# Kernel tuning notes

Hardware: AMD Instinct MI355X
Metric: run time of the kernel (lower is better)

## Reference

```python
import jax, jax.numpy as jnp
import numpy as np

D_MODEL, D_HEAD, N_HEAD, PERIOD = 1024, 64, 16, 30
B, T1, T2 = 2, 2048, 2048


def setup_inputs() -> dict:
    key = jax.random.key(0)
    ks = jax.random.split(key, 7)
    s_in = 1.0 / np.sqrt(D_MODEL)
    s_out = 1.0 / np.sqrt(N_HEAD * D_HEAD)
    return {
        "x": jax.random.normal(ks[0], (B, T1, D_MODEL), dtype=jnp.float32),
        "context": jax.random.normal(ks[1], (B, T2, D_MODEL), dtype=jnp.float32),
        "Wq": jax.random.uniform(ks[2], (N_HEAD * D_HEAD, D_MODEL), jnp.float32, -s_in, s_in),
        "Wk": jax.random.uniform(ks[3], (N_HEAD * D_HEAD, D_MODEL), jnp.float32, -s_in, s_in),
        "Wv": jax.random.uniform(ks[4], (N_HEAD * D_HEAD, D_MODEL), jnp.float32, -s_in, s_in),
        "Wo": jax.random.uniform(ks[5], (D_MODEL, N_HEAD * D_HEAD), jnp.float32, -s_out, s_out),
        "bo": jax.random.uniform(ks[6], (D_MODEL,), jnp.float32, -s_out, s_out),
    }


def reference(x, context, Wq, Wk, Wv, Wo, bo):
    Bx, T1x, _ = x.shape
    T2x = context.shape[1]
    scale = 1.0 / np.sqrt(D_HEAD).astype(np.float32)
    # projections (torch Linear: y = x @ W^T)
    q = (x @ Wq.T).reshape(Bx, T1x, N_HEAD, D_HEAD)
    k = (context @ Wk.T).reshape(Bx, T2x, N_HEAD, D_HEAD)
    v = (context @ Wv.T).reshape(Bx, T2x, N_HEAD, D_HEAD)
    # attention scores [B, H, T1, T2]
    scores = jnp.einsum('bihd,bjhd->bhij', q, k) * scale
    # ALiBi-style periodic distance bias
    dist = jnp.abs(jnp.arange(T1x)[:, None] - jnp.arange(T2x)[None, :])  # [T1,T2]
    bias = -(dist // PERIOD).astype(jnp.float32)                          # [T1,T2]
    head_scale = jnp.power(2.0, -jnp.arange(1, N_HEAD + 1, dtype=jnp.float32))
    biased = scores + bias[None, None, :, :] * head_scale[None, :, None, None]
    attn = jax.nn.softmax(biased, axis=-1)
    out = jnp.einsum('bhij,bjhd->bihd', attn, v).reshape(Bx, T1x, N_HEAD * D_HEAD)
    # output projection; dropout is identity in eval mode
    return out @ Wo.T + bo
```

## Files before the change

### kernel.cpp

```cpp
#include <hip/hip_runtime.h>
#include <hip/hip_fp16.h>

typedef _Float16 f16;
typedef __attribute__((ext_vector_type(8))) _Float16 f16x8;
typedef __attribute__((ext_vector_type(4))) _Float16 f16x4;
typedef __attribute__((ext_vector_type(2))) __fp16 fp16x2;
typedef __attribute__((ext_vector_type(4))) float f32x4;
typedef __attribute__((ext_vector_type(16))) float f32x16;

#define DM 1024
#define NH 16
#define DH 64
#define TT 2048
#define LOG2E 1.4426950408889634f
#define QSCALE 0.18033688f

__device__ __forceinline__ void gl16(const void* g, void* l) {
  __builtin_amdgcn_global_load_lds((const __attribute__((address_space(1))) void*)g,
                                   (__attribute__((address_space(3))) void*)l, 16, 0, 0);
}

#define SB0 __builtin_amdgcn_sched_barrier(0)
#define LGKM0 asm volatile("s_waitcnt lgkmcnt(0)" ::: "memory")

__global__ __launch_bounds__(256) void cvt_all(const float* __restrict__ x, const float* __restrict__ cx,
                                               const float* __restrict__ wq, const float* __restrict__ wk,
                                               const float* __restrict__ wv, const float* __restrict__ wo,
                                               f16* __restrict__ xb, f16* __restrict__ cb,
                                               f16* __restrict__ wqb, f16* __restrict__ wkb,
                                               f16* __restrict__ wvb, f16* __restrict__ wob,
                                               f16* __restrict__ FBf) {
  int idx = blockIdx.x * 256 + threadIdx.x;
  int stride = gridDim.x * 256;
  for (int i = idx; i < 3670016; i += stride) {
    if (i >= 3145728) {
      int c = i - 3145728;
      int half = c & 1, lane = (c >> 1) & 63, kvt = (c >> 7) & 63, qt = c >> 13;
      int qi = qt * 32 + (lane & 31);
      int jb = kvt * 32 + 16 * half + 8 * (lane >> 5);
      f16x8 v;
#pragma unroll
      for (int e = 0; e < 8; e++) {
        int d = qi - (jb + e); d = (d < 0) ? -d : d;
        v[e] = (f16)(d / 30);
      }
      reinterpret_cast<f16x8*>(FBf)[c] = v;
      continue;
    }
    const float* src; f16* dst; int off; float s = 1.0f;
    if (i < 2097152) {
      if (i < 1048576) { src = x; dst = xb; off = i; }
      else { src = cx; dst = cb; off = i - 1048576; }
    } else {
      int j = i - 2097152;
      int wsel = j >> 18;
      off = j & 262143;
      if (wsel == 0) { src = wq; dst = wqb; s = QSCALE; }
      else if (wsel == 1) { src = wk; dst = wkb; }
      else if (wsel == 2) { src = wv; dst = wvb; }
      else { src = wo; dst = wob; }
    }
    float4 v = reinterpret_cast<const float4*>(src)[off];
    f16x4 o = { (f16)(v.x * s), (f16)(v.y * s), (f16)(v.z * s), (f16)(v.w * s) };
    reinterpret_cast<f16x4*>(dst)[off] = o;
  }
}

__device__ __forceinline__ void gemm_mainloop(const f16* __restrict__ A, const f16* __restrict__ W,
                                              int bm, int bn, f16 (*As)[4096], f16 (*Bs)[4096],
                                              f32x4 (&acc)[4][4]) {
  int t = threadIdx.x;
  int w = t >> 6;
  int lane = t & 63, lr = lane & 15, g = lane >> 4;
  int wr = w >> 1, wc = w & 1;
  int scol = ((t & 3) ^ ((t >> 3) & 3)) * 8;
  const f16* a0 = A + (size_t)(bm + (t >> 2)) * DM + scol;
  const f16* b0 = W + (size_t)(bn + (t >> 2)) * DM + scol;
  int wo = w * 512;
  int szg = ((lr >> 1) & 3) << 4;

  auto STG = [&](int bufi, int kt) {
    gl16(a0 + kt, As[bufi] + wo);
    gl16(a0 + kt + (size_t)64 * DM, As[bufi] + 2048 + wo);
    gl16(b0 + kt, Bs[bufi] + wo);
    gl16(b0 + kt + (size_t)64 * DM, Bs[bufi] + 2048 + wo);
  };

  STG(0, 0);
  __syncthreads();
  int buf = 0;
  for (int kt = 0; kt < DM; kt += 32) {
    if (kt + 32 < DM) STG(buf ^ 1, kt + 32);
    const char* Ab = (const char*)As[buf];
    const char* Bb = (const char*)Bs[buf];
    f16x8 af[4], bf[4];
#pragma unroll
    for (int mi = 0; mi < 4; mi++) {
      int row = wr * 64 + mi * 16 + lr;
      af[mi] = *reinterpret_cast<const f16x8*>(Ab + row * 64 + ((g << 4) ^ szg));
    }
#pragma unroll
    for (int ni = 0; ni < 4; ni++) {
      int row = wc * 64 + ni * 16 + lr;
      bf[ni] = *reinterpret_cast<const f16x8*>(Bb + row * 64 + ((g << 4) ^ szg));
    }
    __builtin_amdgcn_s_setprio(1);
#pragma unroll
    for (int mi = 0; mi < 4; mi++)
#pragma unroll
      for (int ni = 0; ni < 4; ni++)
        acc[mi][ni] = __builtin_amdgcn_mfma_f32_16x16x32_f16(af[mi], bf[ni], acc[mi][ni], 0, 0, 0);
    __builtin_amdgcn_s_setprio(0);
    __syncthreads();
    buf ^= 1;
  }
}

__global__ __launch_bounds__(256) void qkv_gemm(const f16* __restrict__ xb, const f16* __restrict__ cb,
                                                const f16* __restrict__ wq, const f16* __restrict__ wk,
                                                const f16* __restrict__ wv,
                                                f16* __restrict__ Qo, f16* __restrict__ Ko,
                                                f16* __restrict__ Vt) {
  __shared__ f16 As[2][4096];
  __shared__ f16 Bs[2][4096];
  int gid = blockIdx.x >> 8;
  int bid = blockIdx.x & 255;
  int bm = (bid >> 3) * 128, bn = (bid & 7) * 128;
  const f16* A = (gid == 0) ? xb : cb;
  const f16* W = (gid == 0) ? wq : ((gid == 1) ? wk : wv);
  f32x4 acc[4][4] = {};
  gemm_mainloop(A, W, bm, bn, As, Bs, acc);

  int t = threadIdx.x, w = t >> 6, lane = t & 63, lr = lane & 15, g = lane >> 4;
  int wr = w >> 1, wc = w & 1;
  if (gid < 2) {
    f16* out = (gid == 0) ? Qo : Ko;
#pragma unroll
    for (int mi = 0; mi < 4; mi++) {
      int m0 = bm + wr * 64 + mi * 16 + 4 * g;
      int b = m0 >> 11, i0 = m0 & 2047;
#pragma unroll
      for (int ni = 0; ni < 4; ni++) {
        int n = bn + wc * 64 + ni * 16 + lr;
        int h = n >> 6, d = n & 63;
        size_t base = (((size_t)(b * NH + h)) * TT + i0) * DH + d;
#pragma unroll
        for (int r = 0; r < 4; r++)
          out[base + (size_t)r * DH] = (f16)acc[mi][ni][r];
      }
    }
  } else {
#pragma unroll
    for (int mi = 0; mi < 4; mi++) {
      int m0 = bm + wr * 64 + mi * 16 + 4 * g;
      int b = m0 >> 11, j0 = m0 & 2047;
#pragma unroll
      for (int ni = 0; ni < 4; ni++) {
        int n = bn + wc * 64 + ni * 16 + lr;
        int h = n >> 6, d = n & 63;
        f16x4 pk = { (f16)acc[mi][ni][0], (f16)acc[mi][ni][1],
                     (f16)acc[mi][ni][2], (f16)acc[mi][ni][3] };
        *reinterpret_cast<f16x4*>(&Vt[(((size_t)(b * NH + h)) * DH + d) * TT + j0]) = pk;
      }
    }
  }
}

__global__ __launch_bounds__(256) void out_gemm(const f16* __restrict__ Ob, const f16* __restrict__ wo,
                                                const float* __restrict__ bo, float* __restrict__ Y) {
  __shared__ f16 As[2][4096];
  __shared__ f16 Bs[2][4096];
  int bid = blockIdx.x;
  int bm = (bid >> 3) * 128, bn = (bid & 7) * 128;
  f32x4 acc[4][4] = {};
  gemm_mainloop(Ob, wo, bm, bn, As, Bs, acc);
  int t = threadIdx.x, w = t >> 6, lane = t & 63, lr = lane & 15, g = lane >> 4;
  int wr = w >> 1, wc = w & 1;
#pragma unroll
  for (int mi = 0; mi < 4; mi++) {
    int m0 = bm + wr * 64 + mi * 16 + 4 * g;
#pragma unroll
    for (int ni = 0; ni < 4; ni++) {
      int n = bn + wc * 64 + ni * 16 + lr;
      float bias = bo[n];
#pragma unroll
      for (int r = 0; r < 4; r++)
        Y[(size_t)(m0 + r) * DM + n] = acc[mi][ni][r] + bias;
    }
  }
}

struct FB4 { f16x8 a, b, c, d; };

__global__ __launch_bounds__(256, 2) void attn_kernel(const f16* __restrict__ Q, const f16* __restrict__ K,
                                                      const f16* __restrict__ V, const f16* __restrict__ FBf,
                                                      f16* __restrict__ O) {
  __shared__ f16 KV[2][8192];
  int o = blockIdx.x;
  int xcd = o & 7, idx = o >> 3;
  int bh = 4 * xcd + (idx >> 4), qblk = idx & 15;
  int h = bh & 15, b = bh >> 4;
  int tt = threadIdx.x, w = tt >> 6, lane = tt & 63;
  int col = lane & 31, hi = lane >> 5;
  int qi = qblk * 128 + w * 32 + col;

  const f16* qp = Q + ((size_t)bh * TT + qi) * DH + hi * 8;
  f16x8 qf[4];
#pragma unroll
  for (int s = 0; s < 4; s++) qf[s] = *reinterpret_cast<const f16x8*>(qp + 16 * s);

  const float nc2 = -exp2f(-(float)(h + 1)) * LOG2E;
  int qtp = qblk * 4 + w;
  const f16x8* fbp = reinterpret_cast<const f16x8*>(FBf) + ((size_t)qtp << 13) + (lane << 1);

  f32x4 rsv = { 0.f, 0.f, 0.f, 0.f };
  f32x16 oacc0 = {}, oacc1 = {};

  int rho0 = tt >> 3, G = tt & 7;
  int f0 = (rho0 & 7) ^ (3 * ((rho0 >> 4) & 1));
  int J0 = (rho0 & 19) | ((rho0 & 4) << 1) | ((rho0 & 8) >> 1);
  const f16* kp0 = K + ((size_t)bh * TT + J0) * DH + (G ^ f0) * 8;
  const f16* kp1 = K + ((size_t)bh * TT + 32 + J0) * DH + (G ^ f0) * 8;
  const f16* vp0 = V + ((size_t)bh * DH + rho0) * TT + (G ^ f0) * 8;
  const f16* vp1 = V + ((size_t)bh * DH + 32 + rho0) * TT + (G ^ f0) * 8;

  f16x8 r0, r1, r2, r3;
  auto LOADR = [&](int kv0) {
    r0 = *reinterpret_cast<const f16x8*>(kp0 + (size_t)kv0 * DH);
    r1 = *reinterpret_cast<const f16x8*>(kp1 + (size_t)kv0 * DH);
    r2 = *reinterpret_cast<const f16x8*>(vp0 + kv0);
    r3 = *reinterpret_cast<const f16x8*>(vp1 + kv0);
  };
  auto WRITE = [&](int bufi) {
    char* base = (char*)KV[bufi];
    *reinterpret_cast<f16x8*>(base + tt * 16) = r0;
    *reinterpret_cast<f16x8*>(base + 4096 + tt * 16) = r1;
    *reinterpret_cast<f16x8*>(base + 8192 + tt * 16) = r2;
    *reinterpret_cast<f16x8*>(base + 12288 + tt * 16) = r3;
  };

  int fcol = (col & 7) ^ (3 * ((col >> 4) & 1));
  int kb0 = col * 128;
  int ksw[4];
#pragma unroll
  for (int s = 0; s < 4; s++) ksw[s] = ((2 * s + hi) ^ fcol) << 4;

  auto FBLOAD = [&](int t) {
    FB4 f;
    f.a = fbp[256 * t];
    f.b = fbp[256 * t + 1];
    f.c = fbp[256 * t + 128];
    f.d = fbp[256 * t + 129];
    return f;
  };

  auto CMP = [&](int bufi, const FB4& fb) {
    const char* Kb = (const char*)KV[bufi];
    f32x16 S0 = {}, S1 = {};
    __builtin_amdgcn_s_setprio(1);
#pragma unroll
    for (int s = 0; s < 4; s++) {
      f16x8 ka0 = *reinterpret_cast<const f16x8*>(Kb + kb0 + ksw[s]);
      f16x8 ka1 = *reinterpret_cast<const f16x8*>(Kb + 4096 + kb0 + ksw[s]);
      S0 = __builtin_amdgcn_mfma_f32_32x32x16_f16(ka0, qf[s], S0, 0, 0, 0);
      S1 = __builtin_amdgcn_mfma_f32_32x32x16_f16(ka1, qf[s], S1, 0, 0, 0);
    }
    __builtin_amdgcn_s_setprio(0);
    float p0[16], p1[16];
#pragma unroll
    for (int r = 0; r < 16; r++) {
      float fb0 = (float)((r < 8) ? fb.a[r] : fb.b[r - 8]);
      float fb1 = (float)((r < 8) ? fb.c[r] : fb.d[r - 8]);
      p0[r] = __builtin_amdgcn_exp2f(fmaf(fb0, nc2, S0[r]));
      p1[r] = __builtin_amdgcn_exp2f(fmaf(fb1, nc2, S1[r]));
    }
#pragma unroll
    for (int r = 0; r < 4; r++) {
      f32x4 pa = { p0[4 * r], p0[4 * r + 1], p0[4 * r + 2], p0[4 * r + 3] };
      f32x4 pc = { p1[4 * r], p1[4 * r + 1], p1[4 * r + 2], p1[4 * r + 3] };
      rsv += pa + pc;
    }
    f16x8 pb[4];
#pragma unroll
    for (int s2 = 0; s2 < 2; s2++) {
      union { f16x8 v; fp16x2 hh[4]; } u0, u1;
#pragma unroll
      for (int q2 = 0; q2 < 4; q2++) {
        u0.hh[q2] = __builtin_amdgcn_cvt_pkrtz(p0[8 * s2 + 2 * q2], p0[8 * s2 + 2 * q2 + 1]);
        u1.hh[q2] = __builtin_amdgcn_cvt_pkrtz(p1[8 * s2 + 2 * q2], p1[8 * s2 + 2 * q2 + 1]);
      }
      pb[s2] = u0.v; pb[2 + s2] = u1.v;
    }
    __builtin_amdgcn_s_setprio(1);
#pragma unroll
    for (int s2 = 0; s2 < 4; s2++) {
      f16x8 va0 = *reinterpret_cast<const f16x8*>(Kb + 8192 + kb0 + ksw[s2]);
      f16x8 va1 = *reinterpret_cast<const f16x8*>(Kb + 12288 + kb0 + ksw[s2]);
      oacc0 = __builtin_amdgcn_mfma_f32_32x32x16_f16(va0, pb[s2], oacc0, 0, 0, 0);
      oacc1 = __builtin_amdgcn_mfma_f32_32x32x16_f16(va1, pb[s2], oacc1, 0, 0, 0);
    }
    __builtin_amdgcn_s_setprio(0);
  };

  LOADR(0);
  WRITE(0);
  LOADR(64);
  FB4 fA = FBLOAD(0);
  FB4 fB = FBLOAD(1);
  LGKM0;
  __builtin_amdgcn_s_barrier();
  SB0;

#pragma unroll 1
  for (int tp = 0; tp < 16; tp++) {
    int t0 = 2 * tp;
    CMP(0, fA);
    WRITE(1);
    if (t0 + 2 < 32) { LOADR((t0 + 2) << 6); fA = FBLOAD(t0 + 2); }
    LGKM0;
    __builtin_amdgcn_s_barrier();
    SB0;
    CMP(1, fB);
    if (t0 + 2 < 32) {
      WRITE(0);
      if (t0 + 3 < 32) { LOADR((t0 + 3) << 6); fB = FBLOAD(t0 + 3); }
      LGKM0;
      __builtin_amdgcn_s_barrier();
      SB0;
    }
  }

  float lsum = (rsv[0] + rsv[1]) + (rsv[2] + rsv[3]);
  lsum += __shfl_xor(lsum, 32, 64);
  float inv = __builtin_amdgcn_rcpf(lsum);

  size_t ob = ((size_t)b * TT + qi) * DM + h * DH + 4 * hi;
  const f32x16* oa[2] = { &oacc0, &oacc1 };
#pragma unroll
  for (int db = 0; db < 2; db++)
#pragma unroll
    for (int a = 0; a < 4; a++) {
      f16x4 o4 = { (f16)((*oa[db])[4 * a] * inv),     (f16)((*oa[db])[4 * a + 1] * inv),
                   (f16)((*oa[db])[4 * a + 2] * inv), (f16)((*oa[db])[4 * a + 3] * inv) };
      *reinterpret_cast<f16x4*>(&O[ob + 32 * db + 8 * a]) = o4;
    }
}

extern "C" void kernel_launch(void* const* d_in, const int* in_sizes, int n_in,
                              void* d_out, int out_size, void* d_ws, size_t ws_size,
                              hipStream_t stream) {
  const float* x  = (const float*)d_in[0];
  const float* cx = (const float*)d_in[1];
  const float* Wq = (const float*)d_in[2];
  const float* Wk = (const float*)d_in[3];
  const float* Wv = (const float*)d_in[4];
  const float* Wo = (const float*)d_in[5];
  const float* bo = (const float*)d_in[6];
  float* Y = (float*)d_out;

  const size_t NTOK = (size_t)2 * TT;
  f16* p = (f16*)d_ws;
  f16* xb  = p; p += NTOK * DM;
  f16* cb  = p; p += NTOK * DM;
  f16* wqb = p; p += (size_t)DM * DM;
  f16* wkb = p; p += (size_t)DM * DM;
  f16* wvb = p; p += (size_t)DM * DM;
  f16* wob = p; p += (size_t)DM * DM;
  f16* Qb  = p; p += NTOK * DM;
  f16* Kb  = p; p += NTOK * DM;
  f16* Vtb = p; p += NTOK * DM;
  f16* Ob  = p; p += NTOK * DM;
  f16* FBt = p;

  cvt_all<<<2048, 256, 0, stream>>>(x, cx, Wq, Wk, Wv, Wo, xb, cb, wqb, wkb, wvb, wob, FBt);
  qkv_gemm<<<768, 256, 0, stream>>>(xb, cb, wqb, wkb, wvb, Qb, Kb, Vtb);
  attn_kernel<<<512, 256, 0, stream>>>(Qb, Kb, Vtb, FBt, Ob);
  out_gemm<<<256, 256, 0, stream>>>(Ob, wob, bo, Y);
}
```

Baseline: 127.2 us.

## Split KV tile across wave pairs with 64-query waves and LDS reduction

Each wave now handles 64 queries and half of each 64-key KV tile, instead of 32 queries over the full tile. Each K fragment read from LDS is reused across two query groups, and the V fragments are shared the same way. The precomputed bias table layout is permuted to match the new per-wave key split. Partial outputs and row sums from the two key-halves are combined through LDS at the end, which adds extra syncs. Registers also roughly double for the four output accumulators, which may hurt occupancy at two blocks per CU.

```diff
diff --git a/kernel.cpp b/kernel.cpp
--- a/kernel.cpp
+++ b/kernel.cpp
@@ -35,9 +35,10 @@
   for (int i = idx; i < 3670016; i += stride) {
     if (i >= 3145728) {
       int c = i - 3145728;
-      int half = c & 1, lane = (c >> 1) & 63, kvt = (c >> 7) & 63, qt = c >> 13;
-      int qi = qt * 32 + (lane & 31);
-      int jb = kvt * 32 + 16 * half + 8 * (lane >> 5);
+      int lane = c & 63, half = (c >> 6) & 1, wj = (c >> 7) & 1;
+      int kvt = (c >> 8) & 31, qt32 = c >> 13;
+      int qi = qt32 * 32 + (lane & 31);
+      int jb = kvt * 64 + wj * 32 + half * 16 + 8 * (lane >> 5);
       f16x8 v;
 #pragma unroll
       for (int e = 0; e < 8; e++) {
@@ -190,7 +191,7 @@
   }
 }
 
-struct FB4 { f16x8 a, b, c, d; };
+struct FBq { f16x8 q0h0, q0h1, q1h0, q1h1; };
 
 __global__ __launch_bounds__(256, 2) void attn_kernel(const f16* __restrict__ Q, const f16* __restrict__ K,
                                                       const f16* __restrict__ V, const f16* __restrict__ FBf,
@@ -201,20 +202,25 @@
   int bh = 4 * xcd + (idx >> 4), qblk = idx & 15;
   int h = bh & 15, b = bh >> 4;
   int tt = threadIdx.x, w = tt >> 6, lane = tt & 63;
+  int wq = w >> 1, wj = w & 1;
   int col = lane & 31, hi = lane >> 5;
-  int qi = qblk * 128 + w * 32 + col;
-
-  const f16* qp = Q + ((size_t)bh * TT + qi) * DH + hi * 8;
-  f16x8 qf[4];
-#pragma unroll
-  for (int s = 0; s < 4; s++) qf[s] = *reinterpret_cast<const f16x8*>(qp + 16 * s);
+  int qbase = qblk * 128 + wq * 64;
+
+  const f16* qp0 = Q + ((size_t)bh * TT + qbase + col) * DH + hi * 8;
+  f16x8 qf0[4], qf1[4];
+#pragma unroll
+  for (int s = 0; s < 4; s++) {
+    qf0[s] = *reinterpret_cast<const f16x8*>(qp0 + 16 * s);
+    qf1[s] = *reinterpret_cast<const f16x8*>(qp0 + 32 * DH + 16 * s);
+  }
 
   const float nc2 = -exp2f(-(float)(h + 1)) * LOG2E;
-  int qtp = qblk * 4 + w;
-  const f16x8* fbp = reinterpret_cast<const f16x8*>(FBf) + ((size_t)qtp << 13) + (lane << 1);
-
-  f32x4 rsv = { 0.f, 0.f, 0.f, 0.f };
-  f32x16 oacc0 = {}, oacc1 = {};
+  int qt32 = qblk * 4 + wq * 2;
+  const f16x8* fb0p = reinterpret_cast<const f16x8*>(FBf) + ((size_t)qt32 << 13) + wj * 128 + lane;
+  const f16x8* fb1p = fb0p + 8192;
+
+  f32x4 rsv0 = { 0.f, 0.f, 0.f, 0.f }, rsv1 = { 0.f, 0.f, 0.f, 0.f };
+  f32x16 o00 = {}, o01 = {}, o10 = {}, o11 = {};
 
   int rho0 = tt >> 3, G = tt & 7;
   int f0 = (rho0 & 7) ^ (3 * ((rho0 >> 4) & 1));
@@ -240,37 +246,38 @@
   };
 
   int fcol = (col & 7) ^ (3 * ((col >> 4) & 1));
-  int kb0 = col * 128;
-  int ksw[4];
+  int kjbase = (32 * wj + col) * 128;
+  int ksw[4], vsw[2];
 #pragma unroll
   for (int s = 0; s < 4; s++) ksw[s] = ((2 * s + hi) ^ fcol) << 4;
+#pragma unroll
+  for (int s2 = 0; s2 < 2; s2++) vsw[s2] = ((4 * wj + 2 * s2 + hi) ^ fcol) << 4;
 
   auto FBLOAD = [&](int t) {
-    FB4 f;
-    f.a = fbp[256 * t];
-    f.b = fbp[256 * t + 1];
-    f.c = fbp[256 * t + 128];
-    f.d = fbp[256 * t + 129];
+    FBq f;
+    f.q0h0 = fb0p[t * 256];
+    f.q0h1 = fb0p[t * 256 + 64];
+    f.q1h0 = fb1p[t * 256];
+    f.q1h1 = fb1p[t * 256 + 64];
     return f;
   };
 
-  auto CMP = [&](int bufi, const FB4& fb) {
+  auto CMP = [&](int bufi, const FBq& fb) {
     const char* Kb = (const char*)KV[bufi];
     f32x16 S0 = {}, S1 = {};
     __builtin_amdgcn_s_setprio(1);
 #pragma unroll
     for (int s = 0; s < 4; s++) {
-      f16x8 ka0 = *reinterpret_cast<const f16x8*>(Kb + kb0 + ksw[s]);
-      f16x8 ka1 = *reinterpret_cast<const f16x8*>(Kb + 4096 + kb0 + ksw[s]);
-      S0 = __builtin_amdgcn_mfma_f32_32x32x16_f16(ka0, qf[s], S0, 0, 0, 0);
-      S1 = __builtin_amdgcn_mfma_f32_32x32x16_f16(ka1, qf[s], S1, 0, 0, 0);
+      f16x8 ka = *reinterpret_cast<const f16x8*>(Kb + kjbase + ksw[s]);
+      S0 = __builtin_amdgcn_mfma_f32_32x32x16_f16(ka, qf0[s], S0, 0, 0, 0);
+      S1 = __builtin_amdgcn_mfma_f32_32x32x16_f16(ka, qf1[s], S1, 0, 0, 0);
     }
     __builtin_amdgcn_s_setprio(0);
     float p0[16], p1[16];
 #pragma unroll
     for (int r = 0; r < 16; r++) {
-      float fb0 = (float)((r < 8) ? fb.a[r] : fb.b[r - 8]);
-      float fb1 = (float)((r < 8) ? fb.c[r] : fb.d[r - 8]);
+      float fb0 = (float)((r < 8) ? fb.q0h0[r] : fb.q0h1[r - 8]);
+      float fb1 = (float)((r < 8) ? fb.q1h0[r] : fb.q1h1[r - 8]);
       p0[r] = __builtin_amdgcn_exp2f(fmaf(fb0, nc2, S0[r]));
       p1[r] = __builtin_amdgcn_exp2f(fmaf(fb1, nc2, S1[r]));
     }
@@ -278,9 +285,9 @@
     for (int r = 0; r < 4; r++) {
       f32x4 pa = { p0[4 * r], p0[4 * r + 1], p0[4 * r + 2], p0[4 * r + 3] };
       f32x4 pc = { p1[4 * r], p1[4 * r + 1], p1[4 * r + 2], p1[4 * r + 3] };
-      rsv += pa + pc;
-    }
-    f16x8 pb[4];
+      rsv0 += pa; rsv1 += pc;
+    }
+    f16x8 pb0[2], pb1[2];
 #pragma unroll
     for (int s2 = 0; s2 < 2; s2++) {
       union { f16x8 v; fp16x2 hh[4]; } u0, u1;
@@ -289,15 +296,17 @@
         u0.hh[q2] = __builtin_amdgcn_cvt_pkrtz(p0[8 * s2 + 2 * q2], p0[8 * s2 + 2 * q2 + 1]);
         u1.hh[q2] = __builtin_amdgcn_cvt_pkrtz(p1[8 * s2 + 2 * q2], p1[8 * s2 + 2 * q2 + 1]);
       }
-      pb[s2] = u0.v; pb[2 + s2] = u1.v;
+      pb0[s2] = u0.v; pb1[s2] = u1.v;
     }
     __builtin_amdgcn_s_setprio(1);
 #pragma unroll
-    for (int s2 = 0; s2 < 4; s2++) {
-      f16x8 va0 = *reinterpret_cast<const f16x8*>(Kb + 8192 + kb0 + ksw[s2]);
-      f16x8 va1 = *reinterpret_cast<const f16x8*>(Kb + 12288 + kb0 + ksw[s2]);
-      oacc0 = __builtin_amdgcn_mfma_f32_32x32x16_f16(va0, pb[s2], oacc0, 0, 0, 0);
-      oacc1 = __builtin_amdgcn_mfma_f32_32x32x16_f16(va1, pb[s2], oacc1, 0, 0, 0);
+    for (int s2 = 0; s2 < 2; s2++) {
+      f16x8 va0 = *reinterpret_cast<const f16x8*>(Kb + 8192 + col * 128 + vsw[s2]);
+      f16x8 va1 = *reinterpret_cast<const f16x8*>(Kb + 8192 + (32 + col) * 128 + vsw[s2]);
+      o00 = __builtin_amdgcn_mfma_f32_32x32x16_f16(va0, pb0[s2], o00, 0, 0, 0);
+      o01 = __builtin_amdgcn_mfma_f32_32x32x16_f16(va1, pb0[s2], o01, 0, 0, 0);
+      o10 = __builtin_amdgcn_mfma_f32_32x32x16_f16(va0, pb1[s2], o10, 0, 0, 0);
+      o11 = __builtin_amdgcn_mfma_f32_32x32x16_f16(va1, pb1[s2], o11, 0, 0, 0);
     }
     __builtin_amdgcn_s_setprio(0);
   };
@@ -305,8 +314,8 @@
   LOADR(0);
   WRITE(0);
   LOADR(64);
-  FB4 fA = FBLOAD(0);
-  FB4 fB = FBLOAD(1);
+  FBq fA = FBLOAD(0);
+  FBq fB = FBLOAD(1);
   LGKM0;
   __builtin_amdgcn_s_barrier();
   SB0;
@@ -330,20 +339,59 @@
     }
   }
 
-  float lsum = (rsv[0] + rsv[1]) + (rsv[2] + rsv[3]);
-  lsum += __shfl_xor(lsum, 32, 64);
-  float inv = __builtin_amdgcn_rcpf(lsum);
-
-  size_t ob = ((size_t)b * TT + qi) * DM + h * DH + 4 * hi;
-  const f32x16* oa[2] = { &oacc0, &oacc1 };
-#pragma unroll
-  for (int db = 0; db < 2; db++)
-#pragma unroll
-    for (int a = 0; a < 4; a++) {
-      f16x4 o4 = { (f16)((*oa[db])[4 * a] * inv),     (f16)((*oa[db])[4 * a + 1] * inv),
-                   (f16)((*oa[db])[4 * a + 2] * inv), (f16)((*oa[db])[4 * a + 3] * inv) };
-      *reinterpret_cast<f16x4*>(&O[ob + 32 * db + 8 * a]) = o4;
-    }
+  float ls0 = (rsv0[0] + rsv0[1]) + (rsv0[2] + rsv0[3]);
+  float ls1 = (rsv1[0] + rsv1[1]) + (rsv1[2] + rsv1[3]);
+  ls0 += __shfl_xor(ls0, 32, 64);
+  ls1 += __shfl_xor(ls1, 32, 64);
+
+  __syncthreads();
+  float* red = (float*)KV;
+  if (wj == 1) {
+    int base = wq * 4096 + lane;
+#pragma unroll
+    for (int r = 0; r < 16; r++) {
+      red[base + r * 64] = o00[r];
+      red[base + 1024 + r * 64] = o01[r];
+      red[base + 2048 + r * 64] = o10[r];
+      red[base + 3072 + r * 64] = o11[r];
+    }
+  }
+  __syncthreads();
+  if (wj == 0) {
+    int base = wq * 4096 + lane;
+#pragma unroll
+    for (int r = 0; r < 16; r++) {
+      o00[r] += red[base + r * 64];
+      o01[r] += red[base + 1024 + r * 64];
+      o10[r] += red[base + 2048 + r * 64];
+      o11[r] += red[base + 3072 + r * 64];
+    }
+  }
+  __syncthreads();
+  if (wj == 1 && lane < 32) {
+    red[wq * 64 + col] = ls0;
+    red[wq * 64 + 32 + col] = ls1;
+  }
+  __syncthreads();
+  if (wj == 0) {
+    float L0 = ls0 + red[wq * 64 + col];
+    float L1 = ls1 + red[wq * 64 + 32 + col];
+    float inv0 = __builtin_amdgcn_rcpf(L0);
+    float inv1 = __builtin_amdgcn_rcpf(L1);
+    const f32x16* oa[4] = { &o00, &o01, &o10, &o11 };
+#pragma unroll
+    for (int q2 = 0; q2 < 4; q2++) {
+      int qg = q2 >> 1, db = q2 & 1;
+      float inv = qg ? inv1 : inv0;
+      size_t ob = ((size_t)b * TT + qbase + 32 * qg + col) * DM + h * DH + 32 * db + 4 * hi;
+#pragma unroll
+      for (int a = 0; a < 4; a++) {
+        f16x4 o4 = { (f16)((*oa[q2])[4 * a] * inv),     (f16)((*oa[q2])[4 * a + 1] * inv),
+                     (f16)((*oa[q2])[4 * a + 2] * inv), (f16)((*oa[q2])[4 * a + 3] * inv) };
+        *reinterpret_cast<f16x4*>(&O[ob + 8 * a]) = o4;
+      }
+    }
+  }
 }
 
 extern "C" void kernel_launch(void* const* d_in, const int* in_sizes, int n_in,
```

New measurement: 147.2 us. 1.16x slower.
